# Kernel optimization log

Measured on AMD Instinct MI355X. Metric: run time of the kernel, lower is better.

The kernel has to match this reference:

```python
import jax, jax.numpy as jnp
import numpy as np

B, T = 2, 2048
V, D, H, HS, L = 32000, 512, 8, 64, 4
FF = 4 * D
EPS = 1e-5


def layer_norm(x, g, b):
    mu = jnp.mean(x, axis=-1, keepdims=True)
    var = jnp.mean((x - mu) ** 2, axis=-1, keepdims=True)
    return (x - mu) * jax.lax.rsqrt(var + EPS) * g + b


def setup_inputs() -> dict:
    key = jax.random.key(0)
    ks = iter(jax.random.split(key, 32))
    s = 0.02
    n = lambda shape: jax.random.normal(next(ks), shape, dtype=jnp.float32) * s
    inp = {
        "idx": jax.random.randint(next(ks), (B, T), 0, V),
        "targets": jax.random.randint(next(ks), (B, T), 0, V),
        "tok_emb": n((V, D)),
        "pos_emb": n((T, D)),
        "ln1_g": jnp.ones((L, D)), "ln1_b": jnp.zeros((L, D)),
        "Wq": n((L, H, D, HS)), "Wk": n((L, H, D, HS)), "Wv": n((L, H, D, HS)),
        "Wo": n((L, H * HS, D)), "bo": jnp.zeros((L, D)),
        "ln2_g": jnp.ones((L, D)), "ln2_b": jnp.zeros((L, D)),
        "W1": n((L, D, FF)), "b1": jnp.zeros((L, FF)),
        "W2": n((L, FF, D)), "b2": jnp.zeros((L, D)),
        "lnf_g": jnp.ones((D,)), "lnf_b": jnp.zeros((D,)),
        "Wout": n((D, V)), "bout": jnp.zeros((V,)),
    }
    return inp


def reference(idx, targets, tok_emb, pos_emb, ln1_g, ln1_b, Wq, Wk, Wv, Wo, bo,
              ln2_g, ln2_b, W1, b1, W2, b2, lnf_g, lnf_b, Wout, bout):
    x = tok_emb[idx] + pos_emb[None, :idx.shape[1], :]  # [B,T,D]
    causal = jnp.tril(jnp.ones((T, T), dtype=bool))
    scale = 1.0 / jnp.sqrt(jnp.float32(D))  # NOTE: source divides by sqrt(C)=sqrt(n_embeddings)
    for l in range(L):
        h = layer_norm(x, ln1_g[l], ln1_b[l])
        q = jnp.einsum('btd,hde->bhte', h, Wq[l])
        k = jnp.einsum('btd,hde->bhte', h, Wk[l])
        v = jnp.einsum('btd,hde->bhte', h, Wv[l])
        w = jnp.einsum('bhte,bhse->bhts', q, k) * scale
        w = jnp.where(causal[None, None], w, -jnp.inf)
        w = jax.nn.softmax(w, axis=-1)  # dropout is identity in eval
        attn = jnp.einsum('bhts,bhse->bhte', w, v)
        attn = attn.transpose(0, 2, 1, 3).reshape(x.shape[0], T, H * HS)
        x = x + attn @ Wo[l] + bo[l]
        h2 = layer_norm(x, ln2_g[l], ln2_b[l])
        x = x + jax.nn.relu(h2 @ W1[l] + b1[l]) @ W2[l] + b2[l]
    x = layer_norm(x, lnf_g, lnf_b)
    logits = x @ Wout + bout  # [B,T,V]
    logp = jax.nn.log_softmax(logits, axis=-1)
    tgt_logp = jnp.take_along_axis(logp, targets[..., None], axis=-1)[..., 0]
    loss = -jnp.mean(tgt_logp)
    return loss, logits
```

## Files before the change

kernel.cpp:

```cpp
#include <hip/hip_runtime.h>
#include <hip/hip_bf16.h>
#include <math.h>

#define TT 2048
#define BB 2
#define VV 32000
#define DD 512
#define HH 8
#define HSS 64
#define LL 4
#define FF_ 2048
#define NBLK_V (VV / 128)

using bf16x8 = __attribute__((ext_vector_type(8))) short;
using floatx4 = __attribute__((ext_vector_type(4))) float;

__device__ __forceinline__ ushort f2bf(float f) {
    __hip_bfloat16 b = __float2bfloat16(f);
    return *reinterpret_cast<ushort*>(&b);
}
__device__ __forceinline__ float bf2f(ushort u) {
    union { unsigned int i; float f; } x; x.i = ((unsigned int)u) << 16; return x.f;
}
__device__ __forceinline__ void gload16(const void* g, void* l) {
    __builtin_amdgcn_global_load_lds(
        (const __attribute__((address_space(1))) void*)g,
        (__attribute__((address_space(3))) void*)l, 16, 0, 0);
}

__global__ __launch_bounds__(64)
void embed_kernel(const int* __restrict__ idx, const float* __restrict__ tok,
                  const float* __restrict__ pos, float* __restrict__ x)
{
    int row = blockIdx.x;
    int t = row & (TT - 1);
    int tokid = idx[row];
    int lane = threadIdx.x;
    const float4* tp = (const float4*)(tok + (size_t)tokid * DD);
    const float4* pp = (const float4*)(pos + (size_t)t * DD);
    float4* xp = (float4*)(x + (size_t)row * DD);
    int i0 = lane * 2;
    float4 a = tp[i0],   b4 = pp[i0];
    float4 c = tp[i0+1], d4 = pp[i0+1];
    xp[i0]   = make_float4(a.x + b4.x, a.y + b4.y, a.z + b4.z, a.w + b4.w);
    xp[i0+1] = make_float4(c.x + d4.x, c.y + d4.y, c.z + d4.z, c.w + d4.w);
}

__global__ __launch_bounds__(256)
void ln_kernel(const float* __restrict__ x, const float* __restrict__ g,
               const float* __restrict__ b, ushort* __restrict__ out)
{
    int wave = threadIdx.x >> 6;
    int lane = threadIdx.x & 63;
    int row  = blockIdx.x * 4 + wave;
    const float* xr = x + (size_t)row * DD;
    float4 v0 = *(const float4*)(xr + lane * 8);
    float4 v1 = *(const float4*)(xr + lane * 8 + 4);
    float s = v0.x + v0.y + v0.z + v0.w + v1.x + v1.y + v1.z + v1.w;
    float q = v0.x*v0.x + v0.y*v0.y + v0.z*v0.z + v0.w*v0.w
            + v1.x*v1.x + v1.y*v1.y + v1.z*v1.z + v1.w*v1.w;
    #pragma unroll
    for (int off = 32; off; off >>= 1) {
        s += __shfl_xor(s, off);
        q += __shfl_xor(q, off);
    }
    float mu  = s * (1.0f / DD);
    float var = q * (1.0f / DD) - mu * mu;
    float rs  = rsqrtf(var + 1e-5f);
    float4 g0 = *(const float4*)(g + lane * 8);
    float4 g1 = *(const float4*)(g + lane * 8 + 4);
    float4 b0 = *(const float4*)(b + lane * 8);
    float4 b1 = *(const float4*)(b + lane * 8 + 4);
    union { ushort u[8]; uint4 v; } pk;
    pk.u[0] = f2bf((v0.x - mu) * rs * g0.x + b0.x);
    pk.u[1] = f2bf((v0.y - mu) * rs * g0.y + b0.y);
    pk.u[2] = f2bf((v0.z - mu) * rs * g0.z + b0.z);
    pk.u[3] = f2bf((v0.w - mu) * rs * g0.w + b0.w);
    pk.u[4] = f2bf((v1.x - mu) * rs * g1.x + b1.x);
    pk.u[5] = f2bf((v1.y - mu) * rs * g1.y + b1.y);
    pk.u[6] = f2bf((v1.z - mu) * rs * g1.z + b1.z);
    pk.u[7] = f2bf((v1.w - mu) * rs * g1.w + b1.w);
    *(uint4*)(out + (size_t)row * DD + lane * 8) = pk.v;
}

__global__ __launch_bounds__(256)
void transpose_cvt(const float* __restrict__ in, ushort* __restrict__ out,
                   int N, int K, long inStrideZ, long outStrideZ)
{
    __shared__ float t[64][65];
    in  += (size_t)blockIdx.z * inStrideZ;
    out += (size_t)blockIdx.z * outStrideZ;
    const int n0 = blockIdx.x * 64, k0 = blockIdx.y * 64;
    const int r = threadIdx.x >> 2;
    const int c = (threadIdx.x & 3) * 16;
    #pragma unroll
    for (int j = 0; j < 16; j += 4) {
        float4 v = *(const float4*)&in[(size_t)(k0 + r) * N + n0 + c + j];
        t[r][c + j + 0] = v.x; t[r][c + j + 1] = v.y;
        t[r][c + j + 2] = v.z; t[r][c + j + 3] = v.w;
    }
    __syncthreads();
    union { ushort u[8]; uint4 v; } pk;
    ushort* orow = out + (size_t)(n0 + r) * K + k0 + c;
    #pragma unroll
    for (int half = 0; half < 2; ++half) {
        #pragma unroll
        for (int j = 0; j < 8; ++j) pk.u[j] = f2bf(t[c + half * 8 + j][r]);
        *(uint4*)(orow + half * 8) = pk.v;
    }
}

__global__ __launch_bounds__(256)
void qkv_transpose(const float* __restrict__ Wq, const float* __restrict__ Wk,
                   const float* __restrict__ Wv, ushort* __restrict__ out)
{
    __shared__ float t[64][65];
    const int z = blockIdx.y;
    const int sel = z >> 5, l = (z >> 3) & 3, h = z & 7;
    const float* in = (sel == 0 ? Wq : sel == 1 ? Wk : Wv)
                      + (size_t)l * (HH * DD * HSS) + (size_t)h * (DD * HSS);
    ushort* ob = out + (size_t)l * (3 * DD * DD) + (size_t)sel * (DD * DD)
                     + (size_t)h * (HSS * DD);
    const int d0 = blockIdx.x * 64;
    const int r = threadIdx.x >> 2;
    const int c = (threadIdx.x & 3) * 16;
    #pragma unroll
    for (int j = 0; j < 16; j += 4) {
        float4 v = *(const float4*)&in[(size_t)(d0 + r) * HSS + c + j];
        t[r][c + j + 0] = v.x; t[r][c + j + 1] = v.y;
        t[r][c + j + 2] = v.z; t[r][c + j + 3] = v.w;
    }
    __syncthreads();
    union { ushort u[8]; uint4 v; } pk;
    ushort* orow = ob + (size_t)r * DD + d0 + c;
    #pragma unroll
    for (int half = 0; half < 2; ++half) {
        #pragma unroll
        for (int j = 0; j < 8; ++j) pk.u[j] = f2bf(t[c + half * 8 + j][r]);
        *(uint4*)(orow + half * 8) = pk.v;
    }
}

__global__ __launch_bounds__(256)
void v_transpose(const ushort* __restrict__ qkv, ushort* __restrict__ vt)
{
    __shared__ ushort t[64][72];
    const int z = blockIdx.y;
    const int t0 = blockIdx.x * 64;
    const int b = z >> 3, h = z & 7;
    const int tr = threadIdx.x >> 2;
    const int dc = (threadIdx.x & 3) * 16;
    const ushort* src = qkv + ((size_t)(b * TT + t0 + tr)) * 1536 + 1024 + h * HSS + dc;
    *(uint4*)&t[tr][dc]     = *(const uint4*)src;
    *(uint4*)&t[tr][dc + 8] = *(const uint4*)(src + 8);
    __syncthreads();
    const int dr = threadIdx.x >> 2;
    const int tc = (threadIdx.x & 3) * 16;
    ushort* dst = vt + ((size_t)z * 64 + dr) * TT + t0 + tc;
    union { ushort u[8]; uint4 v; } p0, p1;
    #pragma unroll
    for (int j = 0; j < 8; ++j) { p0.u[j] = t[tc + j][dr]; p1.u[j] = t[tc + 8 + j][dr]; }
    *(uint4*)dst       = p0.v;
    *(uint4*)(dst + 8) = p1.v;
}

__global__ __launch_bounds__(512, 2)
void mfma_gemm_logits(const ushort* __restrict__ A, int lda,
                      const ushort* __restrict__ Bt, int ldb,
                      float* __restrict__ Cf, int ldc,
                      const float* __restrict__ bias,
                      int K,
                      float* __restrict__ smax, float* __restrict__ ssum, int nblks)
{
    __shared__ ushort As[32 * 512];
    __shared__ ushort Bs[16 * 512];
    __shared__ float sstat[2][256][2];

    const int bxx = blockIdx.x, byy = blockIdx.y;
    const int m0 = byy << 8, n0 = bxx << 7;
    const int tid = threadIdx.x, w = tid >> 6, lane = tid & 63;
    const int wm = w >> 1, wn = w & 1;
    const int l15 = lane & 15, lk = lane >> 4;

    floatx4 acc[4][4] = {};

    for (int k0 = 0; k0 < K; k0 += 64) {
        #pragma unroll
        for (int i = 0; i < 4; ++i) {
            int c = 4 * w + i;
            int cg = c >> 1, ckh = c & 1;
            gload16(A + (size_t)(m0 + cg * 16 + l15) * lda + k0 + lk * 8 + ckh * 32,
                    &As[c * 512]);
        }
        #pragma unroll
        for (int i = 0; i < 2; ++i) {
            int c = 2 * w + i;
            int cg = c >> 1, ckh = c & 1;
            gload16(Bt + (size_t)(n0 + cg * 16 + l15) * ldb + k0 + lk * 8 + ckh * 32,
                    &Bs[c * 512]);
        }
        __syncthreads();
        #pragma unroll
        for (int kh = 0; kh < 2; ++kh) {
            bf16x8 af[4], bfr[4];
            #pragma unroll
            for (int mi = 0; mi < 4; ++mi)
                af[mi] = *(const bf16x8*)&As[(((wm * 4 + mi) * 2 + kh) * 64 + lane) * 8];
            #pragma unroll
            for (int ni = 0; ni < 4; ++ni)
                bfr[ni] = *(const bf16x8*)&Bs[(((wn * 4 + ni) * 2 + kh) * 64 + lane) * 8];
            #pragma unroll
            for (int mi = 0; mi < 4; ++mi)
                #pragma unroll
                for (int ni = 0; ni < 4; ++ni)
                    acc[mi][ni] = __builtin_amdgcn_mfma_f32_16x16x32_bf16(
                        af[mi], bfr[ni], acc[mi][ni], 0, 0, 0);
        }
        __syncthreads();
    }

    #pragma unroll
    for (int mi = 0; mi < 4; ++mi)
        #pragma unroll
        for (int ni = 0; ni < 4; ++ni) {
            float bv = bias[n0 + wn * 64 + ni * 16 + l15];
            #pragma unroll
            for (int r = 0; r < 4; ++r) acc[mi][ni][r] += bv;
        }

    #pragma unroll
    for (int mi = 0; mi < 4; ++mi) {
        #pragma unroll
        for (int r = 0; r < 4; ++r) {
            int grow = m0 + wm * 64 + mi * 16 + lk * 4 + r;
            #pragma unroll
            for (int ni = 0; ni < 4; ++ni)
                Cf[(size_t)grow * ldc + n0 + wn * 64 + ni * 16 + l15] = acc[mi][ni][r];
        }
    }

    #pragma unroll
    for (int mi = 0; mi < 4; ++mi) {
        #pragma unroll
        for (int r = 0; r < 4; ++r) {
            float m4 = fmaxf(fmaxf(acc[mi][0][r], acc[mi][1][r]),
                             fmaxf(acc[mi][2][r], acc[mi][3][r]));
            m4 = fmaxf(m4, __shfl_xor(m4, 1));
            m4 = fmaxf(m4, __shfl_xor(m4, 2));
            m4 = fmaxf(m4, __shfl_xor(m4, 4));
            m4 = fmaxf(m4, __shfl_xor(m4, 8));
            float s4 = 0.f;
            #pragma unroll
            for (int ni = 0; ni < 4; ++ni) s4 += __expf(acc[mi][ni][r] - m4);
            s4 += __shfl_xor(s4, 1);
            s4 += __shfl_xor(s4, 2);
            s4 += __shfl_xor(s4, 4);
            s4 += __shfl_xor(s4, 8);
            if (l15 == 0) {
                int R = wm * 64 + mi * 16 + lk * 4 + r;
                sstat[0][R][wn] = m4;
                sstat[1][R][wn] = s4;
            }
        }
    }
    __syncthreads();
    if (tid < 256) {
        float ma = sstat[0][tid][0], mb = sstat[0][tid][1];
        float M = fmaxf(ma, mb);
        float S = sstat[1][tid][0] * __expf(ma - M)
                + sstat[1][tid][1] * __expf(mb - M);
        smax[(size_t)(m0 + tid) * nblks + bxx] = M;
        ssum[(size_t)(m0 + tid) * nblks + bxx] = S;
    }
}

__global__ __launch_bounds__(256, 2)
void mfma_gemm_db(const ushort* __restrict__ A, int lda,
                  const ushort* __restrict__ Bt, int ldb,
                  float* __restrict__ Cf, ushort* __restrict__ Cbf, int ldc,
                  const float* __restrict__ bias,
                  const float* __restrict__ resid, int ldres,
                  int K, int relu)
{
    __shared__ ushort st[2][2][8192];

    const int m0 = blockIdx.y << 7, n0 = blockIdx.x << 7;
    const int tid = threadIdx.x, w = tid >> 6, lane = tid & 63;
    const int wm = w >> 1, wn = w & 1;
    const int l15 = lane & 15, lk = lane >> 4;
    const int nt = K >> 6;

    auto STAGE = [&](int t, int p) {
        const int k0 = t << 6;
        #pragma unroll
        for (int i = 0; i < 4; ++i) {
            int c = 4 * w + i;
            int cg = c >> 3, cmi = (c >> 1) & 3, ckh = c & 1;
            gload16(A + (size_t)(m0 + cg * 64 + cmi * 16 + l15) * lda
                      + k0 + lk * 8 + ckh * 32, &st[p][0][c * 512]);
            gload16(Bt + (size_t)(n0 + cg * 64 + cmi * 16 + l15) * ldb
                       + k0 + lk * 8 + ckh * 32, &st[p][1][c * 512]);
        }
    };

    floatx4 acc[4][4] = {};
    STAGE(0, 0);

    for (int t = 0; t < nt; ++t) {
        const int p = t & 1;
        if (t + 1 < nt) {
            STAGE(t + 1, p ^ 1);
            asm volatile("s_waitcnt vmcnt(8)" ::: "memory");
        } else {
            asm volatile("s_waitcnt vmcnt(0)" ::: "memory");
        }
        __builtin_amdgcn_s_barrier();
        __builtin_amdgcn_sched_barrier(0);
        #pragma unroll
        for (int kh = 0; kh < 2; ++kh) {
            bf16x8 af[4], bfr[4];
            #pragma unroll
            for (int mi = 0; mi < 4; ++mi)
                af[mi] = *(const bf16x8*)&st[p][0][((wm * 8 + mi * 2 + kh) * 64 + lane) * 8];
            #pragma unroll
            for (int ni = 0; ni < 4; ++ni)
                bfr[ni] = *(const bf16x8*)&st[p][1][((wn * 8 + ni * 2 + kh) * 64 + lane) * 8];
            #pragma unroll
            for (int mi = 0; mi < 4; ++mi)
                #pragma unroll
                for (int ni = 0; ni < 4; ++ni)
                    acc[mi][ni] = __builtin_amdgcn_mfma_f32_16x16x32_bf16(
                        af[mi], bfr[ni], acc[mi][ni], 0, 0, 0);
        }
        __builtin_amdgcn_sched_barrier(0);
        __builtin_amdgcn_s_barrier();
    }

    #pragma unroll
    for (int mi = 0; mi < 4; ++mi)
        #pragma unroll
        for (int ni = 0; ni < 4; ++ni)
            #pragma unroll
            for (int r = 0; r < 4; ++r) {
                float v = acc[mi][ni][r];
                if (bias) v += bias[n0 + wn * 64 + ni * 16 + l15];
                if (relu) v = fmaxf(v, 0.0f);
                acc[mi][ni][r] = v;
            }

    #pragma unroll
    for (int mi = 0; mi < 4; ++mi) {
        #pragma unroll
        for (int r = 0; r < 4; ++r) {
            int grow = m0 + wm * 64 + mi * 16 + lk * 4 + r;
            #pragma unroll
            for (int ni = 0; ni < 4; ++ni) {
                int gcol = n0 + wn * 64 + ni * 16 + l15;
                float v = acc[mi][ni][r];
                if (resid) v += resid[(size_t)grow * ldres + gcol];
                if (Cbf) Cbf[(size_t)grow * ldc + gcol] = f2bf(v);
                else     Cf [(size_t)grow * ldc + gcol] = v;
            }
        }
    }
}

__global__ __launch_bounds__(256, 3)
void mfma_gemm_db64(const ushort* __restrict__ A, int lda,
                    const ushort* __restrict__ Bt, int ldb,
                    float* __restrict__ Cf, ushort* __restrict__ Cbf, int ldc,
                    const float* __restrict__ bias,
                    const float* __restrict__ resid, int ldres,
                    int K, int relu)
{
    __shared__ ushort stA[2][8 * 512];
    __shared__ ushort stB[2][16 * 512];

    const int m0 = blockIdx.y << 6, n0 = blockIdx.x << 7;
    const int tid = threadIdx.x, w = tid >> 6, lane = tid & 63;
    const int l15 = lane & 15, lk = lane >> 4;
    const int nt = K >> 6;

    auto STAGE = [&](int t, int p) {
        const int k0 = t << 6;
        #pragma unroll
        for (int i = 0; i < 2; ++i) {
            int c = 2 * w + i;
            int cmi = c >> 1, ckh = c & 1;
            gload16(A + (size_t)(m0 + cmi * 16 + l15) * lda
                      + k0 + lk * 8 + ckh * 32, &stA[p][c * 512]);
        }
        #pragma unroll
        for (int i = 0; i < 4; ++i) {
            int c = 4 * w + i;
            int cnj = c >> 1, ckh = c & 1;
            gload16(Bt + (size_t)(n0 + cnj * 16 + l15) * ldb
                       + k0 + lk * 8 + ckh * 32, &stB[p][c * 512]);
        }
    };

    floatx4 acc[4][2] = {};
    STAGE(0, 0);

    for (int t = 0; t < nt; ++t) {
        const int p = t & 1;
        if (t + 1 < nt) {
            STAGE(t + 1, p ^ 1);
            asm volatile("s_waitcnt vmcnt(6)" ::: "memory");
        } else {
            asm volatile("s_waitcnt vmcnt(0)" ::: "memory");
        }
        __builtin_amdgcn_s_barrier();
        __builtin_amdgcn_sched_barrier(0);
        #pragma unroll
        for (int kh = 0; kh < 2; ++kh) {
            bf16x8 af[4], bfr[2];
            #pragma unroll
            for (int mi = 0; mi < 4; ++mi)
                af[mi] = *(const bf16x8*)&stA[p][((mi * 2 + kh) * 64 + lane) * 8];
            #pragma unroll
            for (int ni = 0; ni < 2; ++ni)
                bfr[ni] = *(const bf16x8*)&stB[p][(((w * 2 + ni) * 2 + kh) * 64 + lane) * 8];
            #pragma unroll
            for (int mi = 0; mi < 4; ++mi)
                #pragma unroll
                for (int ni = 0; ni < 2; ++ni)
                    acc[mi][ni] = __builtin_amdgcn_mfma_f32_16x16x32_bf16(
                        af[mi], bfr[ni], acc[mi][ni], 0, 0, 0);
        }
        __builtin_amdgcn_sched_barrier(0);
        __builtin_amdgcn_s_barrier();
    }

    #pragma unroll
    for (int mi = 0; mi < 4; ++mi)
        #pragma unroll
        for (int ni = 0; ni < 2; ++ni)
            #pragma unroll
            for (int r = 0; r < 4; ++r) {
                float v = acc[mi][ni][r];
                if (bias) v += bias[n0 + w * 32 + ni * 16 + l15];
                if (relu) v = fmaxf(v, 0.0f);
                acc[mi][ni][r] = v;
            }

    #pragma unroll
    for (int mi = 0; mi < 4; ++mi) {
        #pragma unroll
        for (int r = 0; r < 4; ++r) {
            int grow = m0 + mi * 16 + lk * 4 + r;
            #pragma unroll
            for (int ni = 0; ni < 2; ++ni) {
                int gcol = n0 + w * 32 + ni * 16 + l15;
                float v = acc[mi][ni][r];
                if (resid) v += resid[(size_t)grow * ldres + gcol];
                if (Cbf) Cbf[(size_t)grow * ldc + gcol] = f2bf(v);
                else     Cf [(size_t)grow * ldc + gcol] = v;
            }
        }
    }
}

__global__ __launch_bounds__(256)
void attn_mfma_kernel(const ushort* __restrict__ qkv, const ushort* __restrict__ vt,
                      ushort* __restrict__ out)
{
    __shared__ ushort Vl[64 * 64];
    __shared__ ushort Pl[64][72];

    const int z = blockIdx.y, b = z >> 3, h = z & 7;
    const int q0 = blockIdx.x << 6;
    const int tid = threadIdx.x;
    const int w = tid >> 6, lane = tid & 63;
    const int l15 = lane & 15, g = lane >> 4;
    const float scale = 0.04419417382415922f;
    const ushort* vbase = vt + (size_t)z * 64 * TT;

    bf16x8 qf0, qf1;
    {
        const ushort* qp = qkv + ((size_t)(b * TT + q0 + 16 * w + l15)) * 1536
                               + h * HSS + g * 8;
        qf0 = *(const bf16x8*)qp;
        qf1 = *(const bf16x8*)(qp + 32);
    }

    bf16x8 kc[8], kn[8];
    {
        #pragma unroll
        for (int kb = 0; kb < 4; ++kb) {
            const ushort* kp = qkv + ((size_t)(b * TT + kb * 16 + l15)) * 1536
                                   + 512 + h * HSS + g * 8;
            kc[kb * 2]     = *(const bf16x8*)kp;
            kc[kb * 2 + 1] = *(const bf16x8*)(kp + 32);
        }
    }

    floatx4 acc_o[4] = {};
    float lreg[4] = {};

    for (int s0 = 0; s0 <= q0; s0 += 64) {
        __syncthreads();
        #pragma unroll
        for (int i = 0; i < 2; ++i) {
            const int cbase = (w * 2 + i) * 64;
            const int c = cbase + lane;
            const int row = c >> 3;
            const int kg = (c & 7) ^ (row & 7);
            gload16(vbase + (size_t)row * TT + s0 + kg * 8, &Vl[cbase * 8]);
        }

        floatx4 s4[4] = {};
        #pragma unroll
        for (int kb = 0; kb < 4; ++kb) {
            s4[kb] = __builtin_amdgcn_mfma_f32_16x16x32_bf16(qf0, kc[kb*2],   s4[kb], 0, 0, 0);
            s4[kb] = __builtin_amdgcn_mfma_f32_16x16x32_bf16(qf1, kc[kb*2+1], s4[kb], 0, 0, 0);
        }

        const bool more = (s0 + 64 <= q0);
        if (more) {
            #pragma unroll
            for (int kb = 0; kb < 4; ++kb) {
                const ushort* kp = qkv + ((size_t)(b * TT + s0 + 64 + kb * 16 + l15)) * 1536
                                       + 512 + h * HSS + g * 8;
                kn[kb * 2]     = *(const bf16x8*)kp;
                kn[kb * 2 + 1] = *(const bf16x8*)(kp + 32);
            }
        }

        const bool diag = (s0 == q0);
        #pragma unroll
        for (int r = 0; r < 4; ++r) {
            const int qrow = q0 + 16 * w + g * 4 + r;
            #pragma unroll
            for (int kb = 0; kb < 4; ++kb) {
                float xs = s4[kb][r] * scale;
                if (diag && (s0 + kb * 16 + l15) > qrow) xs = -1e30f;
                float p = __expf(xs);
                lreg[r] += p;
                Pl[16 * w + g * 4 + r][kb * 16 + l15] = f2bf(p);
            }
        }
        __syncthreads();

        bf16x8 pa0 = *(const bf16x8*)&Pl[16 * w + l15][g * 8];
        bf16x8 pa1 = *(const bf16x8*)&Pl[16 * w + l15][g * 8 + 32];
        #pragma unroll
        for (int db = 0; db < 4; ++db) {
            const int row = db * 16 + l15;
            const bf16x8 vb0 = *(const bf16x8*)&Vl[row * 64 + ((g       ^ (row & 7)) * 8)];
            const bf16x8 vb1 = *(const bf16x8*)&Vl[row * 64 + (((g + 4) ^ (row & 7)) * 8)];
            acc_o[db] = __builtin_amdgcn_mfma_f32_16x16x32_bf16(pa0, vb0, acc_o[db], 0, 0, 0);
            acc_o[db] = __builtin_amdgcn_mfma_f32_16x16x32_bf16(pa1, vb1, acc_o[db], 0, 0, 0);
        }

        if (more) {
            #pragma unroll
            for (int i = 0; i < 8; ++i) kc[i] = kn[i];
        }
    }

    #pragma unroll
    for (int r = 0; r < 4; ++r) {
        float l = lreg[r];
        l += __shfl_xor(l, 1);
        l += __shfl_xor(l, 2);
        l += __shfl_xor(l, 4);
        l += __shfl_xor(l, 8);
        float inv = 1.0f / l;
        ushort* op = out + ((size_t)(b * TT + q0 + 16 * w + g * 4 + r)) * DD + h * HSS;
        #pragma unroll
        for (int db = 0; db < 4; ++db)
            op[db * 16 + l15] = f2bf(acc_o[db][r] * inv);
    }
}

__global__ __launch_bounds__(256)
void rowloss_finalize(const float* __restrict__ logits, const int* __restrict__ targets,
                      const float* __restrict__ smax, const float* __restrict__ ssum,
                      float* __restrict__ rowloss)
{
    const int wv = threadIdx.x >> 6, lane = threadIdx.x & 63;
    const int row = blockIdx.x * 4 + wv;
    const float* mrow = smax + (size_t)row * NBLK_V;
    const float* srow = ssum + (size_t)row * NBLK_V;
    float M = -1e30f;
    for (int i = lane; i < NBLK_V; i += 64) M = fmaxf(M, mrow[i]);
    #pragma unroll
    for (int off = 32; off; off >>= 1) M = fmaxf(M, __shfl_xor(M, off));
    float S = 0.f;
    for (int i = lane; i < NBLK_V; i += 64) S += srow[i] * __expf(mrow[i] - M);
    #pragma unroll
    for (int off = 32; off; off >>= 1) S += __shfl_xor(S, off);
    if (lane == 0)
        rowloss[row] = -(logits[(size_t)row * VV + targets[row]] - M - logf(S));
}

__global__ __launch_bounds__(256)
void loss_finalize(const float* __restrict__ rowloss, float* __restrict__ out)
{
    __shared__ float red[256];
    float s = 0.f;
    for (int i = threadIdx.x; i < BB * TT; i += 256) s += rowloss[i];
    red[threadIdx.x] = s; __syncthreads();
    for (int s2 = 128; s2; s2 >>= 1) {
        if (threadIdx.x < s2) red[threadIdx.x] += red[threadIdx.x + s2];
        __syncthreads();
    }
    if (threadIdx.x == 0) out[0] = red[0] * (1.0f / (BB * TT));
}

extern "C" void kernel_launch(void* const* d_in, const int* in_sizes, int n_in,
                              void* d_out, int out_size, void* d_ws, size_t ws_size,
                              hipStream_t stream) {
    const int*   idx     = (const int*)  d_in[0];
    const int*   targets = (const int*)  d_in[1];
    const float* tok_emb = (const float*)d_in[2];
    const float* pos_emb = (const float*)d_in[3];
    const float* ln1_g   = (const float*)d_in[4];
    const float* ln1_b   = (const float*)d_in[5];
    const float* Wq      = (const float*)d_in[6];
    const float* Wk      = (const float*)d_in[7];
    const float* Wv      = (const float*)d_in[8];
    const float* Wo      = (const float*)d_in[9];
    const float* bo      = (const float*)d_in[10];
    const float* ln2_g   = (const float*)d_in[11];
    const float* ln2_b   = (const float*)d_in[12];
    const float* W1      = (const float*)d_in[13];
    const float* b1      = (const float*)d_in[14];
    const float* W2      = (const float*)d_in[15];
    const float* b2      = (const float*)d_in[16];
    const float* lnf_g   = (const float*)d_in[17];
    const float* lnf_b   = (const float*)d_in[18];
    const float* Wout    = (const float*)d_in[19];
    const float* bout    = (const float*)d_in[20];

    float* outf   = (float*)d_out;
    float* logits = outf + 1;

    const size_t ROW = (size_t)BB * TT;

    float*  x     = (float*)d_ws;
    ushort* h_bf  = (ushort*)(x + ROW * DD);
    ushort* Woutt = h_bf + ROW * DD;
    float*  rowloss = (float*)(Woutt + (size_t)VV * DD);
    float* smax = x;
    float* ssum = x + ROW * NBLK_V;

    ushort* sc     = (ushort*)(outf + 8);
    ushort* qkv_bf = sc;
    ushort* ff_bf  = qkv_bf + ROW * 1536;
    ushort* Wqkvt  = ff_bf + ROW * FF_;
    ushort* Wot    = Wqkvt + (size_t)LL * 1536 * DD;
    ushort* W1t    = Wot   + (size_t)LL * DD * DD;
    ushort* W2t    = W1t   + (size_t)LL * FF_ * DD;
    ushort* vt_g   = W2t   + (size_t)LL * DD * FF_;

    qkv_transpose<<<dim3(8, 96), 256, 0, stream>>>(Wq, Wk, Wv, Wqkvt);
    transpose_cvt<<<dim3(8, 8, LL),  256, 0, stream>>>(Wo,   Wot,   DD,  DD,  (long)DD*DD,   (long)DD*DD);
    transpose_cvt<<<dim3(32, 8, LL), 256, 0, stream>>>(W1,   W1t,   FF_, DD,  (long)DD*FF_,  (long)DD*FF_);
    transpose_cvt<<<dim3(8, 32, LL), 256, 0, stream>>>(W2,   W2t,   DD,  FF_, (long)FF_*DD,  (long)FF_*DD);
    transpose_cvt<<<dim3(500, 8, 1), 256, 0, stream>>>(Wout, Woutt, VV,  DD,  0, 0);

    embed_kernel<<<ROW, 64, 0, stream>>>(idx, tok_emb, pos_emb, x);

    for (int l = 0; l < LL; ++l) {
        ln_kernel<<<ROW / 4, 256, 0, stream>>>(x, ln1_g + l * DD, ln1_b + l * DD, h_bf);

        mfma_gemm_db<<<dim3(1536 / 128, ROW / 128), 256, 0, stream>>>(
            h_bf, DD, Wqkvt + (size_t)l * 1536 * DD, DD,
            nullptr, qkv_bf, 1536, nullptr, nullptr, 0, DD, 0);

        v_transpose<<<dim3(TT / 64, BB * HH), 256, 0, stream>>>(qkv_bf, vt_g);

        attn_mfma_kernel<<<dim3(TT / 64, BB * HH), 256, 0, stream>>>(qkv_bf, vt_g, h_bf);

        mfma_gemm_db64<<<dim3(DD / 128, ROW / 64), 256, 0, stream>>>(
            h_bf, DD, Wot + (size_t)l * DD * DD, DD,
            x, nullptr, DD, bo + l * DD, x, DD, DD, 0);

        ln_kernel<<<ROW / 4, 256, 0, stream>>>(x, ln2_g + l * DD, ln2_b + l * DD, h_bf);

        mfma_gemm_db<<<dim3(FF_ / 128, ROW / 128), 256, 0, stream>>>(
            h_bf, DD, W1t + (size_t)l * FF_ * DD, DD,
            nullptr, ff_bf, FF_, b1 + l * FF_, nullptr, 0, DD, 1);

        mfma_gemm_db64<<<dim3(DD / 128, ROW / 64), 256, 0, stream>>>(
            ff_bf, FF_, W2t + (size_t)l * DD * FF_, FF_,
            x, nullptr, DD, b2 + l * DD, x, DD, FF_, 0);
    }

    ln_kernel<<<ROW / 4, 256, 0, stream>>>(x, lnf_g, lnf_b, h_bf);

    mfma_gemm_logits<<<dim3(VV / 128, ROW / 256), 512, 0, stream>>>(
        h_bf, DD, Woutt, DD,
        logits, VV, bout, DD,
        smax, ssum, NBLK_V);

    rowloss_finalize<<<ROW / 4, 256, 0, stream>>>(logits, targets, smax, ssum, rowloss);
    loss_finalize<<<1, 256, 0, stream>>>(rowloss, outf);
}
```

Before: 1.227 ms.

## Double-buffer LDS tiles in logits GEMM with prefetch of next K-slice

Restructures the logits GEMM main loop to use two LDS buffers with a K-step of 32 instead of a single buffer with K-step 64. The next tile's global-to-LDS loads are issued before computing on the current one, and partial vmcnt waits let the loads overlap with MFMA work. This targets the load latency that previously sat between the two syncthreads in every iteration. The cost is twice as many iterations and barriers, half as much MFMA work per barrier, and reliance on hand-placed waitcnt counts being correct.

Measured after the change: 1.229 ms. No clear change (+0.2%).

```diff
diff --git a/kernel.cpp b/kernel.cpp
--- a/kernel.cpp
+++ b/kernel.cpp
@@ -172,8 +172,8 @@
                       int K,
                       float* __restrict__ smax, float* __restrict__ ssum, int nblks)
 {
-    __shared__ ushort As[32 * 512];
-    __shared__ ushort Bs[16 * 512];
+    __shared__ ushort As[2][16 * 512];
+    __shared__ ushort Bs[2][8 * 512];
     __shared__ float sstat[2][256][2];
 
     const int bxx = blockIdx.x, byy = blockIdx.y;
@@ -181,34 +181,41 @@
     const int tid = threadIdx.x, w = tid >> 6, lane = tid & 63;
     const int wm = w >> 1, wn = w & 1;
     const int l15 = lane & 15, lk = lane >> 4;
+    const int nt = K >> 5;
+
+    auto STAGE = [&](int t, int p) {
+        const int k0 = t << 5;
+        #pragma unroll
+        for (int i = 0; i < 2; ++i) {
+            int cg = 2 * w + i;
+            gload16(A + (size_t)(m0 + cg * 16 + l15) * lda + k0 + lk * 8,
+                    &As[p][cg * 512]);
+        }
+        gload16(Bt + (size_t)(n0 + w * 16 + l15) * ldb + k0 + lk * 8,
+                &Bs[p][w * 512]);
+    };
 
     floatx4 acc[4][4] = {};
-
-    for (int k0 = 0; k0 < K; k0 += 64) {
-        #pragma unroll
-        for (int i = 0; i < 4; ++i) {
-            int c = 4 * w + i;
-            int cg = c >> 1, ckh = c & 1;
-            gload16(A + (size_t)(m0 + cg * 16 + l15) * lda + k0 + lk * 8 + ckh * 32,
-                    &As[c * 512]);
-        }
-        #pragma unroll
-        for (int i = 0; i < 2; ++i) {
-            int c = 2 * w + i;
-            int cg = c >> 1, ckh = c & 1;
-            gload16(Bt + (size_t)(n0 + cg * 16 + l15) * ldb + k0 + lk * 8 + ckh * 32,
-                    &Bs[c * 512]);
-        }
-        __syncthreads();
-        #pragma unroll
-        for (int kh = 0; kh < 2; ++kh) {
+    STAGE(0, 0);
+
+    for (int t = 0; t < nt; ++t) {
+        const int p = t & 1;
+        if (t + 1 < nt) {
+            STAGE(t + 1, p ^ 1);
+            asm volatile("s_waitcnt vmcnt(3)" ::: "memory");
+        } else {
+            asm volatile("s_waitcnt vmcnt(0)" ::: "memory");
+        }
+        __builtin_amdgcn_s_barrier();
+        __builtin_amdgcn_sched_barrier(0);
+        {
             bf16x8 af[4], bfr[4];
             #pragma unroll
             for (int mi = 0; mi < 4; ++mi)
-                af[mi] = *(const bf16x8*)&As[(((wm * 4 + mi) * 2 + kh) * 64 + lane) * 8];
+                af[mi] = *(const bf16x8*)&As[p][((wm * 4 + mi) * 64 + lane) * 8];
             #pragma unroll
             for (int ni = 0; ni < 4; ++ni)
-                bfr[ni] = *(const bf16x8*)&Bs[(((wn * 4 + ni) * 2 + kh) * 64 + lane) * 8];
+                bfr[ni] = *(const bf16x8*)&Bs[p][((wn * 4 + ni) * 64 + lane) * 8];
             #pragma unroll
             for (int mi = 0; mi < 4; ++mi)
                 #pragma unroll
@@ -216,7 +223,8 @@
                     acc[mi][ni] = __builtin_amdgcn_mfma_f32_16x16x32_bf16(
                         af[mi], bfr[ni], acc[mi][ni], 0, 0, 0);
         }
-        __syncthreads();
+        __builtin_amdgcn_sched_barrier(0);
+        __builtin_amdgcn_s_barrier();
     }
 
     #pragma unroll
```
